# Optimization experiments

Measured on AMD Instinct MI355X. Metric: run time of the kernel, lower is better.

## Reference

```python
import jax, jax.numpy as jnp
import numpy as np

N = 8192
E = 262144


def gcn_layer(x, w, row, col, edge_weight, n_nodes):
    # support = x @ W ; out = A_sparse @ support (COO spmm via segment_sum)
    support = x @ w                              # [N, d_out]
    msg = support[col] * edge_weight[:, None]    # gather + scale, [E, d_out]
    return jax.ops.segment_sum(msg, row, num_segments=n_nodes)  # [N, d_out]


def setup_inputs() -> dict:
    key = jax.random.key(0)
    k1, k2, k3, k4, k5, k6 = jax.random.split(key, 6)
    x = jax.random.normal(k1, (N, 512), dtype=jnp.float32)
    w1 = jax.random.normal(k2, (512, 256), dtype=jnp.float32) * 0.05
    w2 = jax.random.normal(k3, (256, 16), dtype=jnp.float32) * 0.05
    edge_weight = jax.random.uniform(k4, (E,), dtype=jnp.float32)
    row = jax.random.randint(k5, (E,), 0, N, dtype=jnp.int32)
    col = jax.random.randint(k6, (E,), 0, N, dtype=jnp.int32)
    return {"x": x, "w1": w1, "w2": w2, "edge_weight": edge_weight,
            "row": row, "col": col}


def reference(x, w1, w2, edge_weight, row, col):
    # gc1: dropout(identity at eval) -> linear -> spmm -> relu
    h1 = jax.nn.relu(gcn_layer(x, w1, row, col, edge_weight, N))
    # gc2: identity activation
    z = gcn_layer(h1, w2, row, col, edge_weight, N)          # [N, 16]
    # InnerProductDecoder with act = identity (dropout off at eval)
    adj = z @ z.T                                            # [N, N]
    return adj
```

## Files before the change

kernel.cpp:

```cpp
#include <hip/hip_runtime.h>

#define NN 8192
#define NE 262144
#define DIN 512
#define DH 256
#define DZ 16

typedef __attribute__((ext_vector_type(8))) short bf16x8;
typedef __attribute__((ext_vector_type(4))) float f32x4;

__device__ __forceinline__ ushort f2bf(float f) {
    uint u = __float_as_uint(f);
    uint r = (u + 0x7FFFu + ((u >> 16) & 1u)) >> 16;
    return (ushort)r;
}
__device__ __forceinline__ float bf2f(ushort h) {
    return __uint_as_float((uint)h << 16);
}

__global__ void k_prep(const float* __restrict__ X, ushort* __restrict__ XBf,
                       const float* __restrict__ W, ushort* __restrict__ WBf,
                       int* __restrict__ cursor) {
    int b = blockIdx.x;
    int t = threadIdx.x;
    if (b < 4096) {
        int i = b * 256 + t;
        float4 v = ((const float4*)X)[i];
        ushort4 h;
        h.x = f2bf(v.x);
        h.y = f2bf(v.y);
        h.z = f2bf(v.z);
        h.w = f2bf(v.w);
        ((ushort4*)XBf)[i] = h;
    } else if (b < 4608) {
        int o = (b - 4096) * 256 + t;
        int n = o >> 9, k = o & 511;
        WBf[o] = f2bf(W[(size_t)k * DH + n]);
    } else {
        cursor[(b - 4608) * 256 + t] = 0;
    }
}

__global__ void k_hist(const int* __restrict__ row, int* __restrict__ cnt) {
    int e = blockIdx.x * blockDim.x + threadIdx.x;
    if (e < NE) atomicAdd(&cnt[row[e]], 1);
}

__global__ __launch_bounds__(1024) void k_scan(const int* __restrict__ cnt,
                                               int* __restrict__ row_ptr,
                                               int* __restrict__ cursor) {
    __shared__ int wsum[16];
    int t = threadIdx.x;
    int wave = t >> 6, lane = t & 63;
    int4 v0 = *(const int4*)&cnt[t * 8];
    int4 v1 = *(const int4*)&cnt[t * 8 + 4];
    int local[8] = {v0.x, v0.y, v0.z, v0.w, v1.x, v1.y, v1.z, v1.w};
    int s = 0;
#pragma unroll
    for (int j = 0; j < 8; j++) s += local[j];
    int si = s;
#pragma unroll
    for (int off = 1; off < 64; off <<= 1) {
        int u = __shfl_up(si, off);
        if (lane >= off) si += u;
    }
    if (lane == 63) wsum[wave] = si;
    __syncthreads();
    if (t < 16) {
        int w = wsum[t];
#pragma unroll
        for (int off = 1; off < 16; off <<= 1) {
            int u = __shfl_up(w, off);
            if (t >= off) w += u;
        }
        wsum[t] = w;
    }
    __syncthreads();
    int base = (wave ? wsum[wave - 1] : 0) + si - s;
#pragma unroll
    for (int j = 0; j < 8; j++) {
        row_ptr[t * 8 + j] = base;
        cursor[t * 8 + j]  = base;
        base += local[j];
    }
    if (t == 1023) row_ptr[NN] = base;
}

__global__ void k_scatter(const int* __restrict__ row, const int* __restrict__ col,
                          const float* __restrict__ ew, int* __restrict__ cursor,
                          int* __restrict__ col_s, float* __restrict__ w_s) {
    int e = blockIdx.x * blockDim.x + threadIdx.x;
    if (e < NE) {
        int r = row[e];
        int pos = atomicAdd(&cursor[r], 1);
        col_s[pos] = col[e];
        w_s[pos]   = ew[e];
    }
}

__global__ __launch_bounds__(256) void k_gemm1_mfma(const ushort* __restrict__ A,
                                                    const ushort* __restrict__ B,
                                                    ushort* __restrict__ O) {
    __shared__ ushort As[64][72];
    __shared__ ushort Bs[64][72];
    int t = threadIdx.x;
    int wave = t >> 6, lane = t & 63;
    int m0 = blockIdx.x * 64, n0 = blockIdx.y * 64;
    int wm = (wave >> 1) * 32, wn = (wave & 1) * 32;
    f32x4 acc[2][2] = {};
    int r0 = t >> 3, c0 = (t & 7) * 8;
    int r1 = r0 + 32;
    int fr = lane & 15, fg = lane >> 4;
    for (int k0 = 0; k0 < DIN; k0 += 64) {
        __syncthreads();
        *(bf16x8*)&As[r0][c0] = *(const bf16x8*)&A[(size_t)(m0 + r0) * DIN + k0 + c0];
        *(bf16x8*)&As[r1][c0] = *(const bf16x8*)&A[(size_t)(m0 + r1) * DIN + k0 + c0];
        *(bf16x8*)&Bs[r0][c0] = *(const bf16x8*)&B[(size_t)(n0 + r0) * DIN + k0 + c0];
        *(bf16x8*)&Bs[r1][c0] = *(const bf16x8*)&B[(size_t)(n0 + r1) * DIN + k0 + c0];
        __syncthreads();
#pragma unroll
        for (int kk = 0; kk < 2; ++kk) {
            bf16x8 af[2], bb[2];
#pragma unroll
            for (int i = 0; i < 2; ++i)
                af[i] = *(const bf16x8*)&As[wm + i * 16 + fr][kk * 32 + fg * 8];
#pragma unroll
            for (int j = 0; j < 2; ++j)
                bb[j] = *(const bf16x8*)&Bs[wn + j * 16 + fr][kk * 32 + fg * 8];
#pragma unroll
            for (int i = 0; i < 2; ++i)
#pragma unroll
                for (int j = 0; j < 2; ++j)
                    acc[i][j] = __builtin_amdgcn_mfma_f32_16x16x32_bf16(
                        af[i], bb[j], acc[i][j], 0, 0, 0);
        }
    }
#pragma unroll
    for (int i = 0; i < 2; ++i)
#pragma unroll
        for (int j = 0; j < 2; ++j)
#pragma unroll
            for (int r = 0; r < 4; ++r)
                O[(size_t)(m0 + wm + i * 16 + fg * 4 + r) * DH + n0 + wn + j * 16 + fr] =
                    f2bf(acc[i][j][r]);
}

__global__ __launch_bounds__(256) void k_spmm1_gemm2(const ushort* __restrict__ Sbf,
                                                     const int* __restrict__ rp,
                                                     const int* __restrict__ cs,
                                                     const float* __restrict__ wsrt,
                                                     const float* __restrict__ W2,
                                                     float* __restrict__ S2) {
    __shared__ float w2s[DH * DZ];
    __shared__ float hs[2][DH];
    int t = threadIdx.x;
#pragma unroll
    for (int i = t; i < DH * DZ / 4; i += 256)
        ((float4*)w2s)[i] = ((const float4*)W2)[i];
    int sub = t >> 7;
    int ht = t & 127;
    int r = blockIdx.x * 2 + sub;
    int e0 = rp[r], e1 = rp[r + 1];
    float a0 = 0.f, a1 = 0.f, b0 = 0.f, b1 = 0.f;
    float c0 = 0.f, c1 = 0.f, d0 = 0.f, d1 = 0.f;
    int e = e0;
    for (; e + 3 < e1; e += 4) {
        int k0 = cs[e], k1 = cs[e + 1], k2 = cs[e + 2], k3 = cs[e + 3];
        float w0 = wsrt[e], w1 = wsrt[e + 1], w2_ = wsrt[e + 2], w3 = wsrt[e + 3];
        uint p0 = *(const uint*)&Sbf[(size_t)k0 * DH + ht * 2];
        uint p1 = *(const uint*)&Sbf[(size_t)k1 * DH + ht * 2];
        uint p2 = *(const uint*)&Sbf[(size_t)k2 * DH + ht * 2];
        uint p3 = *(const uint*)&Sbf[(size_t)k3 * DH + ht * 2];
        a0 += w0 * bf2f((ushort)p0); a1 += w0 * bf2f((ushort)(p0 >> 16));
        b0 += w1 * bf2f((ushort)p1); b1 += w1 * bf2f((ushort)(p1 >> 16));
        c0 += w2_ * bf2f((ushort)p2); c1 += w2_ * bf2f((ushort)(p2 >> 16));
        d0 += w3 * bf2f((ushort)p3); d1 += w3 * bf2f((ushort)(p3 >> 16));
    }
    for (; e < e1; ++e) {
        float w0 = wsrt[e];
        uint p0 = *(const uint*)&Sbf[(size_t)cs[e] * DH + ht * 2];
        a0 += w0 * bf2f((ushort)p0); a1 += w0 * bf2f((ushort)(p0 >> 16));
    }
    float2 o;
    o.x = fmaxf(a0 + b0 + c0 + d0, 0.f);
    o.y = fmaxf(a1 + b1 + c1 + d1, 0.f);
    *(float2*)&hs[sub][ht * 2] = o;
    __syncthreads();
    int j = (t >> 3) & 15, g = t & 7;
    float acc = 0.f;
#pragma unroll
    for (int kk = 0; kk < 32; ++kk) {
        int k = g * 32 + kk;
        acc += hs[sub][k] * w2s[k * DZ + j];
    }
    acc += __shfl_xor(acc, 1);
    acc += __shfl_xor(acc, 2);
    acc += __shfl_xor(acc, 4);
    if (g == 0) S2[(size_t)r * DZ + j] = acc;
}

__global__ __launch_bounds__(256) void k_spmm2(const float* __restrict__ S2,
                                               const int* __restrict__ rp,
                                               const int* __restrict__ cs,
                                               const float* __restrict__ wsrt,
                                               ushort* __restrict__ ZHi,
                                               ushort* __restrict__ ZLo) {
    int t = threadIdx.x;
    int rl = t >> 4, c = t & 15;
    int r = blockIdx.x * 16 + rl;
    int e0 = rp[r], e1 = rp[r + 1];
    float acc = 0.f;
    for (int e = e0; e < e1; ++e) acc += wsrt[e] * S2[(size_t)cs[e] * DZ + c];
    ushort h = f2bf(acc);
    ZHi[(size_t)r * DZ + c] = h;
    ZLo[(size_t)r * DZ + c] = f2bf(acc - bf2f(h));
}

__global__ __launch_bounds__(256) void k_gemm3_mfma(const ushort* __restrict__ ZHi,
                                                    const ushort* __restrict__ ZLo,
                                                    float* __restrict__ O) {
    int t = threadIdx.x;
    int wave = t >> 6, lane = t & 63;
    int rb = blockIdx.y * 128 + (wave >> 1) * 64;
    int cb = blockIdx.x * 128 + (wave & 1) * 64;
    int fr = lane & 15, fg = lane >> 4;
    int ko = (fg & 1) * 8;
    const ushort* asel = (fg < 2) ? ZHi : ZLo;

    bf16x8 cpack[4], rhi[4], rlo[4];
    bf16x8 zero8 = {};
#pragma unroll
    for (int j = 0; j < 4; ++j)
        cpack[j] = *(const bf16x8*)&asel[(size_t)(cb + j * 16 + fr) * DZ + ko];
#pragma unroll
    for (int i = 0; i < 4; ++i) {
        rhi[i] = *(const bf16x8*)&ZHi[(size_t)(rb + i * 16 + fr) * DZ + ko];
        rlo[i] = (fg < 2) ? *(const bf16x8*)&ZLo[(size_t)(rb + i * 16 + fr) * DZ + ko]
                          : zero8;
    }
    f32x4 acc[4][4] = {};
#pragma unroll
    for (int i = 0; i < 4; ++i)
#pragma unroll
        for (int j = 0; j < 4; ++j) {
            acc[i][j] = __builtin_amdgcn_mfma_f32_16x16x32_bf16(cpack[j], rhi[i],
                                                                acc[i][j], 0, 0, 0);
            acc[i][j] = __builtin_amdgcn_mfma_f32_16x16x32_bf16(cpack[j], rlo[i],
                                                                acc[i][j], 0, 0, 0);
        }
#pragma unroll
    for (int i = 0; i < 4; ++i)
#pragma unroll
        for (int j = 0; j < 4; ++j)
            *(f32x4*)&O[(size_t)(rb + i * 16 + fr) * NN + cb + j * 16 + fg * 4] = acc[i][j];
}

extern "C" void kernel_launch(void* const* d_in, const int* in_sizes, int n_in,
                              void* d_out, int out_size, void* d_ws, size_t ws_size,
                              hipStream_t stream) {
    const float* x  = (const float*)d_in[0];
    const float* w1 = (const float*)d_in[1];
    const float* w2 = (const float*)d_in[2];
    const float* ew = (const float*)d_in[3];
    const int*  row = (const int*)d_in[4];
    const int*  col = (const int*)d_in[5];
    float* out = (float*)d_out;

    char* ws = (char*)d_ws;
    int*    row_ptr = (int*)ws;
    int*    cursor  = (int*)(ws + 36864);
    ushort* zhi     = (ushort*)(ws + 73728);
    ushort* zlo     = (ushort*)(ws + 73728 + 262144);

    char* ob = (char*)d_out;
    ushort* support1 = (ushort*)ob;
    float*  s2       = (float*)(ob + 16u * 1024 * 1024);
    int*    col_s    = (int*)(ob + 17u * 1024 * 1024);
    float*  w_s      = (float*)(ob + 18u * 1024 * 1024);
    ushort* xbf      = (ushort*)(ob + 20u * 1024 * 1024);
    ushort* w1tbf    = (ushort*)(ob + 36u * 1024 * 1024);

    k_prep<<<4640, 256, 0, stream>>>(x, xbf, w1, w1tbf, cursor);

    k_hist<<<NE / 256, 256, 0, stream>>>(row, cursor);
    k_scan<<<1, 1024, 0, stream>>>(cursor, row_ptr, cursor);
    k_scatter<<<NE / 256, 256, 0, stream>>>(row, col, ew, cursor, col_s, w_s);

    k_gemm1_mfma<<<dim3(NN / 64, DH / 64), 256, 0, stream>>>(xbf, w1tbf, support1);
    k_spmm1_gemm2<<<NN / 2, 256, 0, stream>>>(support1, row_ptr, col_s, w_s, w2, s2);

    k_spmm2<<<NN / 16, 256, 0, stream>>>(s2, row_ptr, col_s, w_s, zhi, zlo);

    k_gemm3_mfma<<<dim3(NN / 128, NN / 128), 256, 0, stream>>>(zhi, zlo, out);
}
```

Before: 145.2 us.

## Fuse X bf16 conversion into GEMM1 load and merge W-prep with histogram

GEMM1 now reads fp32 X directly and converts it to bf16 while staging the A tile into shared memory, so the separate pass that wrote and re-read a 8 MB bf16 copy of X is gone. The W1 transpose/convert and the row histogram are merged into one launch, and the counter zeroing becomes a memset. The trade-off is that each of the four column-block CTAs of GEMM1 re-reads and re-converts the fp32 X rows, doubling A-side global traffic per tile, and the A load pattern changes to 16 floats per thread.

Result: no change. 147.9 us (+1.9%).

```diff
diff --git a/kernel.cpp b/kernel.cpp
--- a/kernel.cpp
+++ b/kernel.cpp
@@ -18,32 +18,18 @@
     return __uint_as_float((uint)h << 16);
 }
 
-__global__ void k_prep(const float* __restrict__ X, ushort* __restrict__ XBf,
-                       const float* __restrict__ W, ushort* __restrict__ WBf,
-                       int* __restrict__ cursor) {
+__global__ void k_prep_hist(const float* __restrict__ W, ushort* __restrict__ WBf,
+                            const int* __restrict__ row, int* __restrict__ cnt) {
     int b = blockIdx.x;
     int t = threadIdx.x;
-    if (b < 4096) {
-        int i = b * 256 + t;
-        float4 v = ((const float4*)X)[i];
-        ushort4 h;
-        h.x = f2bf(v.x);
-        h.y = f2bf(v.y);
-        h.z = f2bf(v.z);
-        h.w = f2bf(v.w);
-        ((ushort4*)XBf)[i] = h;
-    } else if (b < 4608) {
-        int o = (b - 4096) * 256 + t;
+    if (b < 512) {
+        int o = b * 256 + t;
         int n = o >> 9, k = o & 511;
         WBf[o] = f2bf(W[(size_t)k * DH + n]);
     } else {
-        cursor[(b - 4608) * 256 + t] = 0;
-    }
-}
-
-__global__ void k_hist(const int* __restrict__ row, int* __restrict__ cnt) {
-    int e = blockIdx.x * blockDim.x + threadIdx.x;
-    if (e < NE) atomicAdd(&cnt[row[e]], 1);
+        int e = (b - 512) * 256 + t;
+        atomicAdd(&cnt[row[e]], 1);
+    }
 }
 
 __global__ __launch_bounds__(1024) void k_scan(const int* __restrict__ cnt,
@@ -98,7 +84,7 @@
     }
 }
 
-__global__ __launch_bounds__(256) void k_gemm1_mfma(const ushort* __restrict__ A,
+__global__ __launch_bounds__(256) void k_gemm1_mfma(const float* __restrict__ X,
                                                     const ushort* __restrict__ B,
                                                     ushort* __restrict__ O) {
     __shared__ ushort As[64][72];
@@ -108,13 +94,23 @@
     int m0 = blockIdx.x * 64, n0 = blockIdx.y * 64;
     int wm = (wave >> 1) * 32, wn = (wave & 1) * 32;
     f32x4 acc[2][2] = {};
+    int ar = t >> 2, ac = (t & 3) * 16;
     int r0 = t >> 3, c0 = (t & 7) * 8;
     int r1 = r0 + 32;
     int fr = lane & 15, fg = lane >> 4;
     for (int k0 = 0; k0 < DIN; k0 += 64) {
         __syncthreads();
-        *(bf16x8*)&As[r0][c0] = *(const bf16x8*)&A[(size_t)(m0 + r0) * DIN + k0 + c0];
-        *(bf16x8*)&As[r1][c0] = *(const bf16x8*)&A[(size_t)(m0 + r1) * DIN + k0 + c0];
+        const float* xp = &X[(size_t)(m0 + ar) * DIN + k0 + ac];
+        float4 f0 = *(const float4*)&xp[0];
+        float4 f1 = *(const float4*)&xp[4];
+        float4 f2 = *(const float4*)&xp[8];
+        float4 f3 = *(const float4*)&xp[12];
+        ushort u[16] = {f2bf(f0.x), f2bf(f0.y), f2bf(f0.z), f2bf(f0.w),
+                        f2bf(f1.x), f2bf(f1.y), f2bf(f1.z), f2bf(f1.w),
+                        f2bf(f2.x), f2bf(f2.y), f2bf(f2.z), f2bf(f2.w),
+                        f2bf(f3.x), f2bf(f3.y), f2bf(f3.z), f2bf(f3.w)};
+        *(bf16x8*)&As[ar][ac]     = *(const bf16x8*)&u[0];
+        *(bf16x8*)&As[ar][ac + 8] = *(const bf16x8*)&u[8];
         *(bf16x8*)&Bs[r0][c0] = *(const bf16x8*)&B[(size_t)(n0 + r0) * DIN + k0 + c0];
         *(bf16x8*)&Bs[r1][c0] = *(const bf16x8*)&B[(size_t)(n0 + r1) * DIN + k0 + c0];
         __syncthreads();
@@ -277,16 +273,14 @@
     float*  s2       = (float*)(ob + 16u * 1024 * 1024);
     int*    col_s    = (int*)(ob + 17u * 1024 * 1024);
     float*  w_s      = (float*)(ob + 18u * 1024 * 1024);
-    ushort* xbf      = (ushort*)(ob + 20u * 1024 * 1024);
     ushort* w1tbf    = (ushort*)(ob + 36u * 1024 * 1024);
 
-    k_prep<<<4640, 256, 0, stream>>>(x, xbf, w1, w1tbf, cursor);
-
-    k_hist<<<NE / 256, 256, 0, stream>>>(row, cursor);
+    hipMemsetAsync(cursor, 0, NN * sizeof(int), stream);
+    k_prep_hist<<<1536, 256, 0, stream>>>(w1, w1tbf, row, cursor);
     k_scan<<<1, 1024, 0, stream>>>(cursor, row_ptr, cursor);
     k_scatter<<<NE / 256, 256, 0, stream>>>(row, col, ew, cursor, col_s, w_s);
 
-    k_gemm1_mfma<<<dim3(NN / 64, DH / 64), 256, 0, stream>>>(xbf, w1tbf, support1);
+    k_gemm1_mfma<<<dim3(NN / 64, DH / 64), 256, 0, stream>>>(x, w1tbf, support1);
     k_spmm1_gemm2<<<NN / 2, 256, 0, stream>>>(support1, row_ptr, col_s, w_s, w2, s2);
 
     k_spmm2<<<NN / 16, 256, 0, stream>>>(s2, row_ptr, col_s, w_s, zhi, zlo);
```
